# Performance work log

Measured on AMD Instinct MI355X. Metric: run time of the kernel, lower is better.

Reference implementation:

```python
import jax, jax.numpy as jnp
import numpy as np

INPUT_SIZE = 4096
OUTPUT_SIZE = 4096
N = 6  # LUT fan-in -> 2^N = 64 entries per LUT
BATCH = 2048


def setup_inputs() -> dict:
    key = jax.random.key(0)
    kx, km, kl = jax.random.split(key, 3)
    # binary input bits stored as float32 {0,1}
    x = jax.random.randint(kx, (BATCH, INPUT_SIZE), 0, 2).astype(jnp.float32)
    # 'random' layer mapping: each of the OUTPUT_SIZE LUTs reads N input bit positions
    mapping = jax.random.randint(km, (OUTPUT_SIZE, N), 0, INPUT_SIZE).astype(jnp.int32)
    # LUT weights, uniform in [-1, 1] as in torch init (clamped to [-1,1] anyway)
    luts = jax.random.uniform(kl, (OUTPUT_SIZE, 2 ** N), dtype=jnp.float32) * 2.0 - 1.0
    return {"x": x, "mapping": mapping, "luts": luts}


def _lut_forward(x, mapping, luts):
    # clamp_luts (training-time clamp, applied in-place in torch forward)
    luts = jnp.clip(luts, -1.0, 1.0)
    n = mapping.shape[1]
    # gather the selected input bits: (B, O, n)
    selected = x[:, mapping]
    # pack bits into a LUT address: (B, O)
    powers = (2 ** jnp.arange(n, dtype=jnp.int32)).astype(x.dtype)
    addresses = (selected * powers).sum(axis=-1).astype(jnp.int32)
    # second gather: per-output LUT lookup -> (B, O)
    out = luts[jnp.arange(luts.shape[0], dtype=jnp.int32)[None, :], addresses]
    # STE binarization (forward: hard threshold > 0)
    binary = (out > 0).astype(out.dtype)
    return out + jax.lax.stop_gradient(binary - out) if False else binary  # fwd-only: hard output


def reference(x, mapping, luts):
    return _lut_forward(x, mapping, luts)
```

## Files before the change

kernel.cpp:

```cpp
#include <hip/hip_runtime.h>
#include <stdint.h>


static constexpr int IN    = 4096;
static constexpr int OUTW  = 4096;
static constexpr int BATCH = 2048;

typedef float vfloat2 __attribute__((ext_vector_type(2)));

__global__ __launch_bounds__(512) void fused_kernel(const float* __restrict__ x,
                                                    const int* __restrict__ mapping,
                                                    const float* __restrict__ luts,
                                                    float* __restrict__ out) {
    __shared__ uint32_t sbits[IN];
    __shared__ unsigned long long smask[1024];

    const int bid  = blockIdx.x;
    const int slot = bid >> 3;
    const int g    = (bid & 7) * 8 + (slot >> 2);
    const int cb   = slot & 3;

#pragma unroll
    for (int c = 0; c < 2; ++c) {
        const int m = c * 2048 + threadIdx.x * 4;
        const float* xb = x + ((size_t)g * 32) * IN + m;
        uint32_t v0 = 0, v1 = 0, v2 = 0, v3 = 0;
#pragma unroll
        for (int r = 0; r < 32; ++r) {
            const float4 f = *(const float4*)(xb + (size_t)r * IN);
            v0 |= ((uint32_t)(f.x != 0.0f)) << r;
            v1 |= ((uint32_t)(f.y != 0.0f)) << r;
            v2 |= ((uint32_t)(f.z != 0.0f)) << r;
            v3 |= ((uint32_t)(f.w != 0.0f)) << r;
        }
        *(uint4*)(sbits + m) = make_uint4(v0, v1, v2, v3);
    }

    {
        const int wave  = threadIdx.x >> 6;
        const int lane  = threadIdx.x & 63;
        const int cbase = wave * 128;
        const float* lp = luts + ((size_t)(cb * 1024 + cbase)) * 64 + lane;
#pragma unroll
        for (int i = 0; i < 128; i += 4) {
            const float v0 = lp[(size_t)(i + 0) * 64];
            const float v1 = lp[(size_t)(i + 1) * 64];
            const float v2 = lp[(size_t)(i + 2) * 64];
            const float v3 = lp[(size_t)(i + 3) * 64];
            const unsigned long long m0 = __ballot(v0 > 0.0f);
            const unsigned long long m1 = __ballot(v1 > 0.0f);
            const unsigned long long m2 = __ballot(v2 > 0.0f);
            const unsigned long long m3 = __ballot(v3 > 0.0f);
            if (lane == 0) {
                smask[cbase + i + 0] = m0;
                smask[cbase + i + 1] = m1;
                smask[cbase + i + 2] = m2;
                smask[cbase + i + 3] = m3;
            }
        }
    }
    __syncthreads();

    const int jl = threadIdx.x * 2;
    const int j  = cb * 1024 + jl;
    const int4* mrow = (const int4*)(mapping + (size_t)j * 6);
    const int4 q0 = mrow[0];
    const int4 q1 = mrow[1];
    const int4 q2 = mrow[2];

    const uint32_t w00 = sbits[q0.x], w01 = sbits[q0.y], w02 = sbits[q0.z],
                   w03 = sbits[q0.w], w04 = sbits[q1.x], w05 = sbits[q1.y];
    const uint32_t w10 = sbits[q1.z], w11 = sbits[q1.w], w12 = sbits[q2.x],
                   w13 = sbits[q2.y], w14 = sbits[q2.z], w15 = sbits[q2.w];
    const unsigned long long mk0 = smask[jl];
    const unsigned long long mk1 = smask[jl + 1];

    float* outp = out + ((size_t)g * 32) * OUTW + j;
#pragma unroll
    for (int r = 0; r < 32; ++r) {
        const uint32_t a0 = ((w00 >> r) & 1u)        | (((w01 >> r) & 1u) << 1)
                          | (((w02 >> r) & 1u) << 2) | (((w03 >> r) & 1u) << 3)
                          | (((w04 >> r) & 1u) << 4) | (((w05 >> r) & 1u) << 5);
        const uint32_t a1 = ((w10 >> r) & 1u)        | (((w11 >> r) & 1u) << 1)
                          | (((w12 >> r) & 1u) << 2) | (((w13 >> r) & 1u) << 3)
                          | (((w14 >> r) & 1u) << 4) | (((w15 >> r) & 1u) << 5);
        vfloat2 res;
        res.x = (float)((uint32_t)(mk0 >> a0) & 1u);
        res.y = (float)((uint32_t)(mk1 >> a1) & 1u);
        __builtin_nontemporal_store(res, (vfloat2*)(outp + (size_t)r * OUTW));
    }
}

extern "C" void kernel_launch(void* const* d_in, const int* in_sizes, int n_in,
                              void* d_out, int out_size, void* d_ws, size_t ws_size,
                              hipStream_t stream) {
    const float* x       = (const float*)d_in[0];
    const int*   mapping = (const int*)d_in[1];
    const float* luts    = (const float*)d_in[2];
    float* out = (float*)d_out;
    (void)d_ws; (void)ws_size;

    hipLaunchKernelGGL(fused_kernel, dim3(256), dim3(512), 0, stream,
                       x, mapping, luts, out);
}
```

Before: 99.43 us.

## Split bit-packing across blocks with inter-block flag handoff via workspace

Each batch group of 32 rows is now handled by 8 blocks of 256 threads instead of 4 blocks of 512, so the grid doubles to 512 blocks. Each block packs only its 512-column slice of x into bits and writes it to a global workspace. It then publishes a release flag, spins until all 8 sibling blocks have published, and copies the full packed row into shared memory. This removes the previous redundant work where every column block re-read and re-packed the whole x tile, at the cost of a global round trip and a spin-wait that needs all sibling blocks resident at once. Flags use a fixed magic value that is never reset, so stale flags from an earlier call could let a block read packed bits before its siblings have written them. A naive fallback kernel is added for when the workspace is too small.

```diff
diff --git a/kernel.cpp b/kernel.cpp
--- a/kernel.cpp
+++ b/kernel.cpp
@@ -5,42 +5,46 @@
 static constexpr int IN    = 4096;
 static constexpr int OUTW  = 4096;
 static constexpr int BATCH = 2048;
+static constexpr unsigned long long MAGIC = 0x9E3779B97F4A7C15ULL;
 
 typedef float vfloat2 __attribute__((ext_vector_type(2)));
 
-__global__ __launch_bounds__(512) void fused_kernel(const float* __restrict__ x,
-                                                    const int* __restrict__ mapping,
-                                                    const float* __restrict__ luts,
-                                                    float* __restrict__ out) {
+__global__ __launch_bounds__(256, 2) void lut_fused_kernel(const float* __restrict__ x,
+                                                           const int* __restrict__ mapping,
+                                                           const float* __restrict__ luts,
+                                                           unsigned long long* __restrict__ flags,
+                                                           uint32_t* __restrict__ xbits,
+                                                           float* __restrict__ out) {
     __shared__ uint32_t sbits[IN];
-    __shared__ unsigned long long smask[1024];
+    __shared__ unsigned long long smask[512];
 
-    const int bid  = blockIdx.x;
-    const int slot = bid >> 3;
-    const int g    = (bid & 7) * 8 + (slot >> 2);
-    const int cb   = slot & 3;
+    const int b  = blockIdx.x;
+    const int t  = threadIdx.x;
+    const int gp = b >> 3;
+    const int cb = b & 7;
 
-#pragma unroll
-    for (int c = 0; c < 2; ++c) {
-        const int m = c * 2048 + threadIdx.x * 4;
-        const float* xb = x + ((size_t)g * 32) * IN + m;
-        uint32_t v0 = 0, v1 = 0, v2 = 0, v3 = 0;
+    {
+        const int m0 = cb * 512 + t * 2;
+        const float* xb = x + ((size_t)gp * 32) * IN + m0;
+        uint32_t v0 = 0, v1 = 0;
 #pragma unroll
         for (int r = 0; r < 32; ++r) {
-            const float4 f = *(const float4*)(xb + (size_t)r * IN);
+            const vfloat2 f = __builtin_nontemporal_load((const vfloat2*)(xb + (size_t)r * IN));
             v0 |= ((uint32_t)(f.x != 0.0f)) << r;
             v1 |= ((uint32_t)(f.y != 0.0f)) << r;
-            v2 |= ((uint32_t)(f.z != 0.0f)) << r;
-            v3 |= ((uint32_t)(f.w != 0.0f)) << r;
         }
-        *(uint4*)(sbits + m) = make_uint4(v0, v1, v2, v3);
+        *(uint2*)(xbits + (size_t)gp * IN + m0) = make_uint2(v0, v1);
+    }
+    __threadfence();
+    __syncthreads();
+    if (t == 0) {
+        __hip_atomic_store(&flags[b], MAGIC, __ATOMIC_RELEASE, __HIP_MEMORY_SCOPE_AGENT);
     }
 
     {
-        const int wave  = threadIdx.x >> 6;
-        const int lane  = threadIdx.x & 63;
-        const int cbase = wave * 128;
-        const float* lp = luts + ((size_t)(cb * 1024 + cbase)) * 64 + lane;
+        const int wv = t >> 6, ln = t & 63;
+        const int colbase = cb * 512 + wv * 128;
+        const float* lp = luts + (size_t)colbase * 64 + ln;
 #pragma unroll
         for (int i = 0; i < 128; i += 4) {
             const float v0 = lp[(size_t)(i + 0) * 64];
@@ -51,31 +55,52 @@
             const unsigned long long m1 = __ballot(v1 > 0.0f);
             const unsigned long long m2 = __ballot(v2 > 0.0f);
             const unsigned long long m3 = __ballot(v3 > 0.0f);
-            if (lane == 0) {
-                smask[cbase + i + 0] = m0;
-                smask[cbase + i + 1] = m1;
-                smask[cbase + i + 2] = m2;
-                smask[cbase + i + 3] = m3;
+            if (ln == 0) {
+                smask[wv * 128 + i + 0] = m0;
+                smask[wv * 128 + i + 1] = m1;
+                smask[wv * 128 + i + 2] = m2;
+                smask[wv * 128 + i + 3] = m3;
             }
         }
     }
-    __syncthreads();
 
-    const int jl = threadIdx.x * 2;
-    const int j  = cb * 1024 + jl;
+    const int jloc = t * 2;
+    const int j    = cb * 512 + jloc;
     const int4* mrow = (const int4*)(mapping + (size_t)j * 6);
     const int4 q0 = mrow[0];
     const int4 q1 = mrow[1];
     const int4 q2 = mrow[2];
 
+    if (t == 0) {
+        const unsigned long long* f = flags + (size_t)gp * 8;
+        for (;;) {
+            int ok = 0;
+#pragma unroll
+            for (int c = 0; c < 8; ++c)
+                ok += (__hip_atomic_load(&f[c], __ATOMIC_ACQUIRE, __HIP_MEMORY_SCOPE_AGENT) == MAGIC);
+            if (ok == 8) break;
+            __builtin_amdgcn_s_sleep(2);
+        }
+    }
+    __syncthreads();
+    __builtin_amdgcn_fence(__ATOMIC_ACQUIRE, "agent");
+
+    {
+        const uint4* src = (const uint4*)(xbits + (size_t)gp * IN);
+        uint4* dst = (uint4*)sbits;
+#pragma unroll
+        for (int i = 0; i < 4; ++i) dst[t + i * 256] = src[t + i * 256];
+    }
+    __syncthreads();
+
     const uint32_t w00 = sbits[q0.x], w01 = sbits[q0.y], w02 = sbits[q0.z],
                    w03 = sbits[q0.w], w04 = sbits[q1.x], w05 = sbits[q1.y];
     const uint32_t w10 = sbits[q1.z], w11 = sbits[q1.w], w12 = sbits[q2.x],
                    w13 = sbits[q2.y], w14 = sbits[q2.z], w15 = sbits[q2.w];
-    const unsigned long long mk0 = smask[jl];
-    const unsigned long long mk1 = smask[jl + 1];
+    const unsigned long long mk0 = smask[jloc];
+    const unsigned long long mk1 = smask[jloc + 1];
 
-    float* outp = out + ((size_t)g * 32) * OUTW + j;
+    float* outp = out + ((size_t)gp * 32) * OUTW + j;
 #pragma unroll
     for (int r = 0; r < 32; ++r) {
         const uint32_t a0 = ((w00 >> r) & 1u)        | (((w01 >> r) & 1u) << 1)
@@ -91,6 +116,23 @@
     }
 }
 
+__global__ __launch_bounds__(256) void naive_kernel(const float* __restrict__ x,
+                                                    const int* __restrict__ mapping,
+                                                    const float* __restrict__ luts,
+                                                    float* __restrict__ out) {
+    const int idx = blockIdx.x * 256 + threadIdx.x;
+    if (idx >= BATCH * OUTW) return;
+    const int b = idx >> 12;
+    const int j = idx & (OUTW - 1);
+    const float* xr = x + (size_t)b * IN;
+    int addr = 0;
+#pragma unroll
+    for (int k = 0; k < 6; ++k) {
+        addr |= ((int)(xr[mapping[j * 6 + k]] != 0.0f)) << k;
+    }
+    out[idx] = (luts[j * 64 + addr] > 0.0f) ? 1.0f : 0.0f;
+}
+
 extern "C" void kernel_launch(void* const* d_in, const int* in_sizes, int n_in,
                               void* d_out, int out_size, void* d_ws, size_t ws_size,
                               hipStream_t stream) {
@@ -98,8 +140,16 @@
     const int*   mapping = (const int*)d_in[1];
     const float* luts    = (const float*)d_in[2];
     float* out = (float*)d_out;
-    (void)d_ws; (void)ws_size;
 
-    hipLaunchKernelGGL(fused_kernel, dim3(256), dim3(512), 0, stream,
-                       x, mapping, luts, out);
+    const size_t flags_bytes = 512 * 8;
+    const size_t xbits_bytes = (size_t)64 * IN * 4;
+    if (ws_size >= flags_bytes + xbits_bytes) {
+        unsigned long long* flags = (unsigned long long*)d_ws;
+        uint32_t* xbits = (uint32_t*)((char*)d_ws + flags_bytes);
+        hipLaunchKernelGGL(lut_fused_kernel, dim3(512), dim3(256), 0, stream,
+                           x, mapping, luts, flags, xbits, out);
+    } else {
+        hipLaunchKernelGGL(naive_kernel, dim3((BATCH * OUTW) / 256), dim3(256), 0, stream,
+                           x, mapping, luts, out);
+    }
 }
```

After: 199.1 us. 100% more time.
